# Kernel optimization log

Measured on AMD Instinct MI355X. Metric: run time of the kernel, lower is better.

The kernel has to match this reference:

```python
import jax, jax.numpy as jnp
import numpy as np


def setup_inputs() -> dict:
    key = jax.random.key(0)
    ks = jax.random.split(key, 7)
    B, T, E, H, V = 32, 200, 32, 128, 8000
    s = lambda fan: 1.0 / np.sqrt(fan)
    return {
        "x": jax.random.normal(ks[0], (B, T, E), dtype=jnp.float32),
        "Ww": jax.random.normal(ks[1], (H, H), dtype=jnp.float32) * s(H),
        "Wb": jax.random.normal(ks[2], (H,), dtype=jnp.float32) * s(H),
        "Uw": jax.random.normal(ks[3], (H, E), dtype=jnp.float32) * s(E),
        "Ub": jax.random.normal(ks[4], (H,), dtype=jnp.float32) * s(E),
        "Vw": jax.random.normal(ks[5], (V, H), dtype=jnp.float32) * s(H),
        "Vb": jax.random.normal(ks[6], (V,), dtype=jnp.float32) * s(H),
    }


def reference(x, Ww, Wb, Uw, Ub, Vw, Vb):
    # x: [B, T, E]. Elman RNN: h_t = tanh(W h_{t-1} + b_W + U x_t + b_U); out_t = V h_t + b_V
    B = x.shape[0]
    H = Ww.shape[0]
    h0 = jnp.zeros((B, H), dtype=x.dtype)
    # Precompute input projections for all timesteps at once: [T, B, H]
    ux = jnp.einsum('bte,he->tbh', x, Uw) + Ub + Wb

    def step(h, ux_t):
        h = jnp.tanh(h @ Ww.T + ux_t)
        return h, h

    hidden, hs = jax.lax.scan(step, h0, ux)  # hs: [T, B, H]
    # Output projection applied to all hidden states (same math as per-step V)
    out_seq = jnp.einsum('tbh,vh->btv', hs, Vw) + Vb  # [B, T, V]
    return out_seq, hidden
```

## Files before the change

### kernel.cpp

```cpp
#include <hip/hip_runtime.h>
#include <stdint.h>

typedef short v8s __attribute__((ext_vector_type(8)));
typedef float v4f __attribute__((ext_vector_type(4)));

__device__ __forceinline__ float bf2f(short s) {
    unsigned int u = ((unsigned int)(unsigned short)s) << 16;
    float f; __builtin_memcpy(&f, &u, 4); return f;
}
__device__ __forceinline__ unsigned short f2bf_rne(float f) {
    unsigned int u; __builtin_memcpy(&u, &f, 4);
    return (unsigned short)((u + 0x7FFFu + ((u >> 16) & 1u)) >> 16);
}
__device__ __forceinline__ unsigned short f2bf_rhu(float f) {
    unsigned int u; __builtin_memcpy(&u, &f, 4);
    return (unsigned short)((u + 0x8000u) >> 16);
}
__device__ __forceinline__ unsigned short f2bf_trunc(float f) {
    unsigned int u; __builtin_memcpy(&u, &f, 4);
    return (unsigned short)(u >> 16);
}
__device__ __forceinline__ float tanh_fast(float z) {
    float e = __expf(2.0f * z);
    float r = __builtin_amdgcn_rcpf(e + 1.0f);
    return __builtin_fmaf(-2.0f, r, 1.0f);
}

__global__ __launch_bounds__(256) void ux_kernel(
    const float* __restrict__ x, const float* __restrict__ Uw,
    const float* __restrict__ Ub, const float* __restrict__ Wb,
    float* __restrict__ ux, unsigned* __restrict__ sync) {
    if (blockIdx.x == 0) {
        for (int i = threadIdx.x; i < 864; i += 256) sync[i] = 0;
    }
    int row = blockIdx.x * 2 + (threadIdx.x >> 7);
    int i = threadIdx.x & 127;
    int b = row & 31, t = row >> 5;
    const float* xr = x + (b * 200 + t) * 32;
    const float* ur = Uw + i * 32;
    float acc = 0.f;
#pragma unroll
    for (int e4 = 0; e4 < 8; ++e4) {
        v4f xv = *(const v4f*)(xr + e4 * 4);
        v4f uv = *(const v4f*)(ur + e4 * 4);
#pragma unroll
        for (int j = 0; j < 4; ++j) acc = __builtin_fmaf(xv[j], uv[j], acc);
    }
    ux[row * 128 + i] = acc + Ub[i] + Wb[i];
}

#define RAWBAR asm volatile("s_waitcnt lgkmcnt(0)\n\ts_barrier" ::: "memory")

__global__ __launch_bounds__(512) void fused_kernel(
    const float* __restrict__ Ww, const float* __restrict__ ux,
    short* __restrict__ hs, float* __restrict__ hidden_out,
    const float* __restrict__ Vw, const float* __restrict__ Vb,
    float* __restrict__ out, unsigned* __restrict__ sync) {
    __shared__ alignas(16) short hbuf[2 * 2 * 16 * 136];
    __shared__ unsigned s_ticket;
    const int tid = threadIdx.x;

    if (tid == 0)
        s_ticket = __hip_atomic_fetch_add(sync, 1u, __ATOMIC_RELAXED,
                                          __HIP_MEMORY_SCOPE_AGENT);
    __syncthreads();
    const unsigned ticket = s_ticket;

    const int w = tid >> 6, lane = tid & 63, q = lane >> 4, c = lane & 15;

    if (ticket < 2) {
        char* lds = (char*)hbuf;
        const int b0 = (int)ticket * 16;
        const int col = 16 * w + c;

        for (int i = tid; i < 1088; i += 512)
            ((v8s*)hbuf)[i] = (v8s){0, 0, 0, 0, 0, 0, 0, 0};

        v8s w_hi[4], w_lo[4];
#pragma unroll
        for (int kb = 0; kb < 4; ++kb) {
            const float* p = Ww + col * 128 + 32 * kb + 8 * q;
#pragma unroll
            for (int j = 0; j < 8; ++j) {
                float v = p[j];
                unsigned short hi = f2bf_rne(v);
                w_hi[kb][j] = (short)hi;
                w_lo[kb][j] = (short)f2bf_rne(v - bf2f((short)hi));
            }
        }

        const int rd_base = c * 272 + 16 * q;
        const int wr_base = q * 1088 + col * 2;

        const float* uxp = ux + (b0 + 4 * q) * 128 + col;
        v4f uxA = {uxp[0], uxp[128], uxp[256], uxp[384]};
        v4f uxB = {uxp[4096], uxp[4224], uxp[4352], uxp[4480]};
        uxp += 8192;
        short* hsp = hs + (b0 + 4 * q) * 128 + col;

        __syncthreads();

#define RNN_STEP(RBUF, WBUF, UXS, SYNC)                                             \
    {                                                                               \
        v4f a0 = UXS;                         \
        UXS[0] = uxp[0]; UXS[1] = uxp[128]; UXS[2] = uxp[256]; UXS[3] = uxp[384];   \
        v4f a1 = {0.f, 0.f, 0.f, 0.f}, a2 = a1;                                     \
        _Pragma("unroll") for (int kb = 0; kb < 4; ++kb) {                          \
            v8s ahi = *(const v8s*)(lds + (RBUF)*8704 + kb * 64 + rd_base);         \
            v8s alo = *(const v8s*)(lds + (RBUF)*8704 + 4352 + kb * 64 + rd_base);  \
            a0 = __builtin_amdgcn_mfma_f32_16x16x32_bf16(ahi, w_hi[kb], a0, 0, 0, 0); \
            a1 = __builtin_amdgcn_mfma_f32_16x16x32_bf16(ahi, w_lo[kb], a1, 0, 0, 0); \
            a2 = __builtin_amdgcn_mfma_f32_16x16x32_bf16(alo, w_hi[kb], a2, 0, 0, 0); \
        }                                                                           \
        _Pragma("unroll") for (int r = 0; r < 4; ++r) {                             \
            float z = (a0[r] + a1[r]) + a2[r];                                      \
            float h = tanh_fast(z);                                                 \
            unsigned short hh = f2bf_rhu(h);                                        \
            float rem = h - bf2f((short)hh);                                        \
            unsigned short hl = f2bf_trunc(rem);                                    \
            *(short*)(lds + (WBUF)*8704 + r * 272 + wr_base) = (short)hh;           \
            *(short*)(lds + (WBUF)*8704 + 4352 + r * 272 + wr_base) = (short)hl;    \
            __hip_atomic_store(hsp + r * 128, (short)hh, __ATOMIC_RELAXED,          \
                               __HIP_MEMORY_SCOPE_AGENT);                           \
        }                                                                           \
        uxp += 4096; hsp += 4096;                                                   \
        SYNC;                                                                       \
    }

        for (int it = 0; it < 50; ++it) {
            RNN_STEP(0, 1, uxA, RAWBAR)
            RNN_STEP(1, 0, uxB, RAWBAR)
            RNN_STEP(0, 1, uxA, RAWBAR)
            RNN_STEP(1, 0, uxB, __syncthreads())
            if (tid == 0)
                __hip_atomic_fetch_add(sync + 16 + it * 16, 1u,
                                       __ATOMIC_RELAXED, __HIP_MEMORY_SCOPE_AGENT);
        }
#undef RNN_STEP

#pragma unroll
        for (int r = 0; r < 4; ++r) {
            short hh = *(short*)(lds + r * 272 + wr_base);
            short hl = *(short*)(lds + 4352 + r * 272 + wr_base);
            hidden_out[(b0 + 4 * q + r) * 128 + col] = bf2f(hh) + bf2f(hl);
        }
        return;
    }

    const int cid0 = (int)ticket - 2;
    const int v_tile = cid0 & 31;
    const int g = cid0 >> 5;
    const int v_wave = v_tile * 256 + 32 * w;
    float* ldsF = (float*)hbuf;

    v8s afr[4][2];
#pragma unroll
    for (int kb = 0; kb < 4; ++kb)
#pragma unroll
        for (int vt = 0; vt < 2; ++vt) {
            int vr = v_wave + 16 * vt + c;
            vr = vr < 8000 ? vr : 7999;
            const float* ap = Vw + vr * 128 + 32 * kb + 8 * q;
            v4f p0 = *(const v4f*)ap;
            v4f p1 = *(const v4f*)(ap + 4);
#pragma unroll
            for (int j = 0; j < 4; ++j) {
                afr[kb][vt][j] = (short)f2bf_rne(p0[j]);
                afr[kb][vt][4 + j] = (short)f2bf_rne(p1[j]);
            }
        }
    v4f vbv[2];
#pragma unroll
    for (int vt = 0; vt < 2; ++vt) {
        int v4b = v_wave + 16 * vt + 4 * q;
        vbv[vt] = *(const v4f*)(Vb + (v4b < 8000 ? v4b : 0));
    }
    const int vcol = v_tile * 256 + 4 * lane;
    const bool vok = vcol < 8000;

    auto do_tile = [&](int tb) {
        const int n0 = tb * 128;

        unsigned* flag = sync + 16 + tb * 16;
        if (tid == 0) {
            while (__hip_atomic_load(flag, __ATOMIC_RELAXED,
                                     __HIP_MEMORY_SCOPE_AGENT) < 2u)
                __builtin_amdgcn_s_sleep(32);
        }
        __syncthreads();

        v4f acc[2][8];
#pragma unroll
        for (int a = 0; a < 2; ++a)
#pragma unroll
            for (int b = 0; b < 8; ++b) acc[a][b] = (v4f){0.f, 0.f, 0.f, 0.f};

#pragma unroll
        for (int kb = 0; kb < 4; ++kb) {
#pragma unroll
            for (int nt = 0; nt < 8; ++nt) {
                v8s bfr = *(const v8s*)(hs + (n0 + 16 * nt + c) * 128 + 32 * kb + 8 * q);
                acc[0][nt] = __builtin_amdgcn_mfma_f32_16x16x32_bf16(afr[kb][0], bfr, acc[0][nt], 0, 0, 0);
                acc[1][nt] = __builtin_amdgcn_mfma_f32_16x16x32_bf16(afr[kb][1], bfr, acc[1][nt], 0, 0, 0);
            }
        }

#pragma unroll
        for (int nt = 0; nt < 8; ++nt) {
#pragma unroll
            for (int vt = 0; vt < 2; ++vt) {
                v4f o;
#pragma unroll
                for (int r = 0; r < 4; ++r) o[r] = acc[vt][nt][r] + vbv[vt][r];
                *(v4f*)&ldsF[c * 260 + 32 * w + 16 * vt + 4 * q] = o;
            }
            RAWBAR;
#pragma unroll
            for (int half = 0; half < 2; ++half) {
                int row = w + 8 * half;
                int n = n0 + 16 * nt + row;
                int t = n >> 5, b = n & 31;
                v4f o = *(const v4f*)&ldsF[row * 260 + 4 * lane];
                if (vok)
                    *(v4f*)(out + (size_t)(b * 200 + t) * 8000 + vcol) = o;
            }
            RAWBAR;
        }
    };

    for (int tb = g; tb < 50; tb += 8) do_tile(tb);
    if (cid0 == 30 || cid0 == 31)
        for (int tb = 7; tb < 50; tb += 8) do_tile(tb);
}

extern "C" void kernel_launch(void* const* d_in, const int* in_sizes, int n_in,
                              void* d_out, int out_size, void* d_ws, size_t ws_size,
                              hipStream_t stream) {
    const float* x  = (const float*)d_in[0];
    const float* Ww = (const float*)d_in[1];
    const float* Wb = (const float*)d_in[2];
    const float* Uw = (const float*)d_in[3];
    const float* Ub = (const float*)d_in[4];
    const float* Vw = (const float*)d_in[5];
    const float* Vb = (const float*)d_in[6];
    float* out = (float*)d_out;

    float* ux = (float*)d_ws;
    short* hs = (short*)((char*)d_ws + 3276800);
    unsigned* sync = (unsigned*)((char*)d_ws + 4915200);

    ux_kernel<<<3200, 256, 0, stream>>>(x, Uw, Ub, Wb, ux, sync);
    fused_kernel<<<256, 512, 0, stream>>>(Ww, ux, hs, out + 51200000,
                                          Vw, Vb, out, sync);
}
```

Before: 403.8 us.

## Offload hidden-state global stores to dedicated writer wave in recurrent block

```diff
diff --git a/kernel.cpp b/kernel.cpp
--- a/kernel.cpp
+++ b/kernel.cpp
@@ -51,12 +51,12 @@
 
 #define RAWBAR asm volatile("s_waitcnt lgkmcnt(0)\n\ts_barrier" ::: "memory")
 
-__global__ __launch_bounds__(512) void fused_kernel(
+__global__ __launch_bounds__(1024) void fused_kernel(
     const float* __restrict__ Ww, const float* __restrict__ ux,
     short* __restrict__ hs, float* __restrict__ hidden_out,
     const float* __restrict__ Vw, const float* __restrict__ Vb,
     float* __restrict__ out, unsigned* __restrict__ sync) {
-    __shared__ alignas(16) short hbuf[2 * 2 * 16 * 136];
+    extern __shared__ char dls[];
     __shared__ unsigned s_ticket;
     const int tid = threadIdx.x;
 
@@ -69,38 +69,36 @@
     const int w = tid >> 6, lane = tid & 63, q = lane >> 4, c = lane & 15;
 
     if (ticket < 2) {
-        char* lds = (char*)hbuf;
+        char* lds = dls;
         const int b0 = (int)ticket * 16;
-        const int col = 16 * w + c;
-
-        for (int i = tid; i < 1088; i += 512)
-            ((v8s*)hbuf)[i] = (v8s){0, 0, 0, 0, 0, 0, 0, 0};
-
-        v8s w_hi[4], w_lo[4];
-#pragma unroll
-        for (int kb = 0; kb < 4; ++kb) {
-            const float* p = Ww + col * 128 + 32 * kb + 8 * q;
-#pragma unroll
-            for (int j = 0; j < 8; ++j) {
-                float v = p[j];
-                unsigned short hi = f2bf_rne(v);
-                w_hi[kb][j] = (short)hi;
-                w_lo[kb][j] = (short)f2bf_rne(v - bf2f((short)hi));
-            }
-        }
-
-        const int rd_base = c * 272 + 16 * q;
-        const int wr_base = q * 1088 + col * 2;
-
-        const float* uxp = ux + (b0 + 4 * q) * 128 + col;
-        v4f uxA = {uxp[0], uxp[128], uxp[256], uxp[384]};
-        v4f uxB = {uxp[4096], uxp[4224], uxp[4352], uxp[4480]};
-        uxp += 8192;
-        short* hsp = hs + (b0 + 4 * q) * 128 + col;
-
+
+        for (int i = tid; i < 1088; i += 1024)
+            ((v8s*)lds)[i] = (v8s){0, 0, 0, 0, 0, 0, 0, 0};
         __syncthreads();
 
-#define RNN_STEP(RBUF, WBUF, UXS, SYNC)                                             \
+        if (w < 8) {
+            const int col = 16 * w + c;
+            v8s w_hi[4], w_lo[4];
+#pragma unroll
+            for (int kb = 0; kb < 4; ++kb) {
+                const float* p = Ww + col * 128 + 32 * kb + 8 * q;
+#pragma unroll
+                for (int j = 0; j < 8; ++j) {
+                    float v = p[j];
+                    unsigned short hi = f2bf_rne(v);
+                    w_hi[kb][j] = (short)hi;
+                    w_lo[kb][j] = (short)f2bf_rne(v - bf2f((short)hi));
+                }
+            }
+            const int rd_base = c * 272 + 16 * q;
+            const int wr_base = q * 1088 + col * 2;
+
+            const float* uxp = ux + (b0 + 4 * q) * 128 + col;
+            v4f uxA = {uxp[0], uxp[128], uxp[256], uxp[384]};
+            v4f uxB = {uxp[4096], uxp[4224], uxp[4352], uxp[4480]};
+            uxp += 8192;
+
+#define RNN_STEP(RBUF, WBUF, UXS)                                                   \
     {                                                                               \
         v4f a0 = UXS;                         \
         UXS[0] = uxp[0]; UXS[1] = uxp[128]; UXS[2] = uxp[256]; UXS[3] = uxp[384];   \
@@ -120,38 +118,85 @@
             unsigned short hl = f2bf_trunc(rem);                                    \
             *(short*)(lds + (WBUF)*8704 + r * 272 + wr_base) = (short)hh;           \
             *(short*)(lds + (WBUF)*8704 + 4352 + r * 272 + wr_base) = (short)hl;    \
-            __hip_atomic_store(hsp + r * 128, (short)hh, __ATOMIC_RELAXED,          \
-                               __HIP_MEMORY_SCOPE_AGENT);                           \
         }                                                                           \
-        uxp += 4096; hsp += 4096;                                                   \
-        SYNC;                                                                       \
-    }
-
-        for (int it = 0; it < 50; ++it) {
-            RNN_STEP(0, 1, uxA, RAWBAR)
-            RNN_STEP(1, 0, uxB, RAWBAR)
-            RNN_STEP(0, 1, uxA, RAWBAR)
-            RNN_STEP(1, 0, uxB, __syncthreads())
-            if (tid == 0)
-                __hip_atomic_fetch_add(sync + 16 + it * 16, 1u,
-                                       __ATOMIC_RELAXED, __HIP_MEMORY_SCOPE_AGENT);
-        }
+        uxp += 4096;                                                                \
+        RAWBAR;                                                                     \
+    }
+
+            for (int it = 0; it < 100; ++it) {
+                RNN_STEP(0, 1, uxA)
+                RNN_STEP(1, 0, uxB)
+            }
 #undef RNN_STEP
 
 #pragma unroll
-        for (int r = 0; r < 4; ++r) {
-            short hh = *(short*)(lds + r * 272 + wr_base);
-            short hl = *(short*)(lds + 4352 + r * 272 + wr_base);
-            hidden_out[(b0 + 4 * q + r) * 128 + col] = bf2f(hh) + bf2f(hl);
+            for (int r = 0; r < 4; ++r) {
+                short hh = *(short*)(lds + r * 272 + wr_base);
+                short hl = *(short*)(lds + 4352 + r * 272 + wr_base);
+                hidden_out[(b0 + 4 * q + r) * 128 + col] = bf2f(hh) + bf2f(hl);
+            }
+        } else if (w == 8) {
+            for (int s = 0; s < 200; ++s) {
+                if (s >= 5 && ((s - 5) & 3) == 0) {
+                    asm volatile("s_waitcnt vmcnt(0)" ::: "memory");
+                    if (lane == 0)
+                        __hip_atomic_fetch_add(sync + 16 + ((s - 5) >> 2) * 16, 1u,
+                                               __ATOMIC_RELAXED,
+                                               __HIP_MEMORY_SCOPE_AGENT);
+                }
+                if (s >= 1) {
+                    const char* src = lds + ((s & 1) ? 8704 : 0);
+#pragma unroll
+                    for (int jj = 0; jj < 4; ++jj) {
+                        int row = 4 * jj + (lane >> 4);
+                        const unsigned long long* p = (const unsigned long long*)
+                            (src + row * 272 + (lane & 15) * 16);
+                        unsigned long long v0 = p[0], v1 = p[1];
+                        unsigned long long* d = (unsigned long long*)
+                            (hs + (s - 1) * 4096 + (b0 + row) * 128 + (lane & 15) * 8);
+                        __hip_atomic_store(d, v0, __ATOMIC_RELAXED,
+                                           __HIP_MEMORY_SCOPE_AGENT);
+                        __hip_atomic_store(d + 1, v1, __ATOMIC_RELAXED,
+                                           __HIP_MEMORY_SCOPE_AGENT);
+                    }
+                }
+                RAWBAR;
+            }
+            {
+                const char* src = lds;
+#pragma unroll
+                for (int jj = 0; jj < 4; ++jj) {
+                    int row = 4 * jj + (lane >> 4);
+                    const unsigned long long* p = (const unsigned long long*)
+                        (src + row * 272 + (lane & 15) * 16);
+                    unsigned long long v0 = p[0], v1 = p[1];
+                    unsigned long long* d = (unsigned long long*)
+                        (hs + 199 * 4096 + (b0 + row) * 128 + (lane & 15) * 8);
+                    __hip_atomic_store(d, v0, __ATOMIC_RELAXED,
+                                       __HIP_MEMORY_SCOPE_AGENT);
+                    __hip_atomic_store(d + 1, v1, __ATOMIC_RELAXED,
+                                       __HIP_MEMORY_SCOPE_AGENT);
+                }
+                asm volatile("s_waitcnt vmcnt(0)" ::: "memory");
+                if (lane == 0) {
+                    __hip_atomic_fetch_add(sync + 16 + 49 * 16, 1u,
+                                           __ATOMIC_RELAXED,
+                                           __HIP_MEMORY_SCOPE_AGENT);
+                }
+            }
+        } else {
+            for (int s = 0; s < 200; ++s) RAWBAR;
         }
         return;
     }
 
-    const int cid0 = (int)ticket - 2;
-    const int v_tile = cid0 & 31;
-    const int g = cid0 >> 5;
-    const int v_wave = v_tile * 256 + 32 * w;
-    float* ldsF = (float*)hbuf;
+    const int half = w >> 3;
+    const int wl = w & 7;
+    const int hcid = ((int)ticket - 2) * 2 + half;
+    const int v_tile = hcid & 31;
+    const int g = hcid >> 5;
+    const int v_wave = v_tile * 256 + 32 * wl;
+    float* ldsF = (float*)(dls + half * 16640);
 
     v8s afr[4][2];
 #pragma unroll
@@ -180,7 +225,6 @@
 
     auto do_tile = [&](int tb) {
         const int n0 = tb * 128;
-
         unsigned* flag = sync + 16 + tb * 16;
         if (tid == 0) {
             while (__hip_atomic_load(flag, __ATOMIC_RELAXED,
@@ -212,12 +256,12 @@
                 v4f o;
 #pragma unroll
                 for (int r = 0; r < 4; ++r) o[r] = acc[vt][nt][r] + vbv[vt][r];
-                *(v4f*)&ldsF[c * 260 + 32 * w + 16 * vt + 4 * q] = o;
+                *(v4f*)&ldsF[c * 260 + 32 * wl + 16 * vt + 4 * q] = o;
             }
             RAWBAR;
 #pragma unroll
-            for (int half = 0; half < 2; ++half) {
-                int row = w + 8 * half;
+            for (int h2 = 0; h2 < 2; ++h2) {
+                int row = wl + 8 * h2;
                 int n = n0 + 16 * nt + row;
                 int t = n >> 5, b = n & 31;
                 v4f o = *(const v4f*)&ldsF[row * 260 + 4 * lane];
@@ -229,7 +273,7 @@
     };
 
     for (int tb = g; tb < 50; tb += 8) do_tile(tb);
-    if (cid0 == 30 || cid0 == 31)
+    if (hcid == 30 || hcid == 31)
         for (int tb = 7; tb < 50; tb += 8) do_tile(tb);
 }
 
@@ -250,6 +294,6 @@
     unsigned* sync = (unsigned*)((char*)d_ws + 4915200);
 
     ux_kernel<<<3200, 256, 0, stream>>>(x, Uw, Ub, Wb, ux, sync);
-    fused_kernel<<<256, 512, 0, stream>>>(Ww, ux, hs, out + 51200000,
-                                          Vw, Vb, out, sync);
-}
+    fused_kernel<<<129, 1024, 81920, stream>>>(Ww, ux, hs, out + 51200000,
+                                               Vw, Vb, out, sync);
+}
```

After: 832.3 us. +106.1%, slower.
